# Kernel optimization log

Measured on AMD Instinct MI355X. Metric: run time of the kernel, lower is better.

The kernel has to match this reference:

```python
import jax, jax.numpy as jnp
import numpy as np

B, M, IN_DIM, D, H, NL = 4, 2048, 512, 1024, 4, 2
HD = D // H           # head_dim = 256
HD2 = HD // 2
ROPE_BASE = 10000.0
LN_EPS = 1e-5


def setup_inputs() -> dict:
    key = jax.random.key(0)
    ks = jax.random.split(key, 9)
    s = 0.02
    return {
        "x": jax.random.normal(ks[0], (B, M, IN_DIM), jnp.float32),
        "positions": jnp.sort(jax.random.randint(ks[1], (B, M), 0, 8192), axis=-1).astype(jnp.int32),
        "mask": jnp.ones((B, M), jnp.float32),
        "in_w": jax.random.normal(ks[2], (IN_DIM, D), jnp.float32) * s,
        "in_b": jnp.zeros((D,), jnp.float32),
        "qkv_w": jax.random.normal(ks[3], (NL, D, 3 * D), jnp.float32) * s,
        "o_w": jax.random.normal(ks[4], (NL, D, D), jnp.float32) * s,
        "ln1_g": jnp.ones((NL, D), jnp.float32),
        "ln1_b": jnp.zeros((NL, D), jnp.float32),
        "ffn_w1": jax.random.normal(ks[5], (NL, D, 4 * D), jnp.float32) * s,
        "ffn_b1": jnp.zeros((NL, 4 * D), jnp.float32),
        "ffn_w2": jax.random.normal(ks[6], (NL, 4 * D, D), jnp.float32) * s,
        "ffn_b2": jnp.zeros((NL, D), jnp.float32),
        "ln2_g": jnp.ones((NL, D), jnp.float32),
        "ln2_b": jnp.zeros((NL, D), jnp.float32),
        "start_state": jax.random.normal(ks[7], (D,), jnp.float32) * 0.02,
    }


def _layernorm(x, g, b):
    mu = jnp.mean(x, axis=-1, keepdims=True)
    var = jnp.mean((x - mu) ** 2, axis=-1, keepdims=True)
    return (x - mu) * jax.lax.rsqrt(var + LN_EPS) * g + b


def _rope_cos_sin(positions):
    # rope_module(pos): angles over head_dim//2 freqs, shared across heads
    inv_freq = 1.0 / (ROPE_BASE ** (jnp.arange(HD2, dtype=jnp.float32) * 2.0 / HD))
    ang = positions.astype(jnp.float32)[:, :, None] * inv_freq  # (B, L, HD2)
    return jnp.cos(ang), jnp.sin(ang)


def _apply_rotary(x, cos, sin):
    # x: (B, H, L, HD); cos/sin: (B, 1, L, HD2) broadcast over heads
    x1, x2 = x[..., :HD2], x[..., HD2:]
    return jnp.concatenate([x1 * cos - x2 * sin, x1 * sin + x2 * cos], axis=-1)


def _self_attention(x, cos, sin, mask, qkv_w, o_w):
    Bx, L, Dx = x.shape
    qkv = (x @ qkv_w).reshape(Bx, L, 3, H, HD)
    q = jnp.transpose(qkv[:, :, 0], (0, 2, 1, 3))  # (B, H, L, HD)
    k = jnp.transpose(qkv[:, :, 1], (0, 2, 1, 3))
    v = jnp.transpose(qkv[:, :, 2], (0, 2, 1, 3))
    q = _apply_rotary(q, cos, sin)
    k = _apply_rotary(k, cos, sin)
    scores = jnp.einsum("bhqd,bhkd->bhqk", q, k) * (1.0 / np.sqrt(HD))
    scores = jnp.where(mask[:, None, None, :] == 0, -jnp.inf, scores)
    attn = jax.nn.softmax(scores, axis=-1)
    out = jnp.einsum("bhqk,bhkd->bhqd", attn, v)
    out = jnp.transpose(out, (0, 2, 1, 3)).reshape(Bx, L, Dx)
    return out @ o_w


def reference(x, positions, mask, in_w, in_b, qkv_w, o_w, ln1_g, ln1_b,
              ffn_w1, ffn_b1, ffn_w2, ffn_b2, ln2_g, ln2_b, start_state):
    h = x @ in_w + in_b  # (B, M, D)
    cos, sin = _rope_cos_sin(positions)
    cos, sin = cos[:, None], sin[:, None]  # (B, 1, M, HD2)
    for l in range(NL):
        h = h + _self_attention(_layernorm(h, ln1_g[l], ln1_b[l]), cos, sin, mask,
                                qkv_w[l], o_w[l])
        y = _layernorm(h, ln2_g[l], ln2_b[l])
        y = jax.nn.gelu(y @ ffn_w1[l] + ffn_b1[l], approximate=False) @ ffn_w2[l] + ffn_b2[l]
        h = h + y
    lengths = jnp.sum(mask, axis=1)
    last_idx = jnp.clip(lengths.astype(jnp.int32) - 1, 0, None)
    gathered = h[jnp.arange(h.shape[0]), last_idx]  # (B, D)
    has_hist = lengths > 0
    return jnp.where(has_hist[:, None], gathered, start_state[None, :])
```

## Files before the change

### kernel.cpp

```cpp
#include <hip/hip_runtime.h>
#include <math.h>

typedef __attribute__((ext_vector_type(8))) short bf16x8;
typedef __attribute__((ext_vector_type(4))) float floatx4;
typedef __attribute__((ext_vector_type(4))) unsigned short ushort4v;

typedef __attribute__((address_space(1))) void as1_void;
typedef __attribute__((address_space(3))) void as3_void;

static __device__ __forceinline__ unsigned short f2b(float f) {
    union { float f; unsigned u; } v; v.f = f;
    unsigned r = v.u + 0x7fffu + ((v.u >> 16) & 1u);
    return (unsigned short)(r >> 16);
}
static __device__ __forceinline__ float b2f(unsigned short h) {
    union { unsigned u; float f; } v; v.u = ((unsigned)h) << 16;
    return v.f;
}

template<int T>
__global__ __launch_bounds__(256) void gemm_bf16(
    const unsigned short* __restrict__ A,
    const unsigned short* __restrict__ Bt,
    float* __restrict__ Cf, unsigned short* __restrict__ Cb,
    const float* __restrict__ bias,
    int K, int lda, int ldb, int ldc,
    int zdiv, long a_s1, long a_s2, long b_s1, long b_s2, long c_s1, long c_s2,
    int mode)
{
    constexpr int F  = T / 32;
    constexpr int NR = T / 64;

    __shared__ unsigned short As[3][4 * T * 8];
    __shared__ unsigned short Bs[3][4 * T * 8];

    const int tid  = threadIdx.x;
    const int wid  = tid >> 6;
    const int lane = tid & 63;
    const int q    = lane >> 4;
    const int r    = lane & 15;

    const int z  = blockIdx.z;
    const int zq = z / zdiv, zr = z % zdiv;
    const long offC = (long)zq * c_s1 + (long)zr * c_s2;

    const int m0 = blockIdx.y * T;
    const int n0 = blockIdx.x * T;

    const unsigned short* Ab = A  + (long)zq * a_s1 + (long)zr * a_s2 + (long)m0 * lda;
    const unsigned short* Bb = Bt + (long)zq * b_s1 + (long)zr * b_s2 + (long)n0 * ldb;

    const int wr = (wid >> 1) * (T / 2);
    const int wc = (wid & 1)  * (T / 2);

    floatx4 acc[F][F];
    #pragma unroll
    for (int i = 0; i < F; ++i)
        #pragma unroll
        for (int j = 0; j < F; ++j)
            acc[i][j] = (floatx4){0.f, 0.f, 0.f, 0.f};

    const int qc = wid;
    const int nk = K >> 5;

    auto stage = [&](int kt, int buf) {
        const int kofs = (kt << 5) + (qc << 3);
        #pragma unroll
        for (int rb = 0; rb < NR; ++rb)
            __builtin_amdgcn_global_load_lds(
                (as1_void*)(void*)(Ab + (long)(lane + rb * 64) * lda + kofs),
                (as3_void*)&As[buf][(qc * T + rb * 64) * 8], 16, 0, 0);
        #pragma unroll
        for (int rb = 0; rb < NR; ++rb)
            __builtin_amdgcn_global_load_lds(
                (as1_void*)(void*)(Bb + (long)(lane + rb * 64) * ldb + kofs),
                (as3_void*)&Bs[buf][(qc * T + rb * 64) * 8], 16, 0, 0);
    };

    stage(0, 0);
    if (nk > 1) stage(1, 1);

    int cur = 0, stb = 2;
    for (int kt = 0; kt < nk; ++kt) {
        if (kt + 1 < nk) {
            if constexpr (NR == 2) asm volatile("s_waitcnt vmcnt(4)" ::: "memory");
            else                   asm volatile("s_waitcnt vmcnt(2)" ::: "memory");
        } else {
            asm volatile("s_waitcnt vmcnt(0)" ::: "memory");
        }
        asm volatile("s_barrier" ::: "memory");
        if (kt + 2 < nk) stage(kt + 2, stb);

        bf16x8 av[F], bv[F];
        #pragma unroll
        for (int i = 0; i < F; ++i)
            av[i] = *(const bf16x8*)&As[cur][(q * T + wr + i * 16 + r) * 8];
        #pragma unroll
        for (int j = 0; j < F; ++j)
            bv[j] = *(const bf16x8*)&Bs[cur][(q * T + wc + j * 16 + r) * 8];
        #pragma unroll
        for (int i = 0; i < F; ++i)
            #pragma unroll
            for (int j = 0; j < F; ++j)
                acc[i][j] = __builtin_amdgcn_mfma_f32_16x16x32_bf16(av[i], bv[j], acc[i][j], 0, 0, 0);

        cur = (cur == 2) ? 0 : cur + 1;
        stb = (stb == 2) ? 0 : stb + 1;
    }

    #pragma unroll
    for (int i = 0; i < F; ++i) {
        const int gr0 = m0 + wr + i * 16 + q * 4;
        #pragma unroll
        for (int j = 0; j < F; ++j) {
            const int gc = n0 + wc + j * 16 + r;
            const float bvl = bias ? bias[gc] : 0.0f;
            #pragma unroll
            for (int rr = 0; rr < 4; ++rr) {
                const long cidx = offC + (long)(gr0 + rr) * ldc + gc;
                float v = acc[i][j][rr] + bvl;
                if (mode == 0) {
                    Cf[cidx] = v;
                } else if (mode == 1) {
                    Cf[cidx] += v;
                } else if (mode == 2) {
                    Cb[cidx] = f2b(v);
                } else {
                    Cb[cidx] = f2b(0.5f * v * (1.0f + erff(v * 0.70710678118654752f)));
                }
            }
        }
    }
}

__global__ void transpose_cast_f32(const float* __restrict__ in, unsigned short* __restrict__ out,
                                   int R, int C)
{
    __shared__ float t[32][33];
    const int c0 = blockIdx.x * 32, r0 = blockIdx.y * 32;
    const int tx = threadIdx.x, ty = threadIdx.y;
    #pragma unroll
    for (int i = 0; i < 4; ++i)
        t[ty + i * 8][tx] = in[(long)(r0 + ty + i * 8) * C + c0 + tx];
    __syncthreads();
    #pragma unroll
    for (int i = 0; i < 4; ++i)
        out[(long)(c0 + ty + i * 8) * R + r0 + tx] = f2b(t[tx][ty + i * 8]);
}

__global__ void transpose_v(const unsigned short* __restrict__ qkv, unsigned short* __restrict__ vT)
{
    __shared__ unsigned short t[32][33];
    const int hh = blockIdx.z;
    const int d0 = blockIdx.x * 32, m0 = blockIdx.y * 32;
    const int tx = threadIdx.x, ty = threadIdx.y;
    const unsigned short* ip = qkv + 2048 + hh * 256;
    unsigned short* op = vT + (long)hh * 524288;
    #pragma unroll
    for (int i = 0; i < 4; ++i)
        t[ty + i * 8][tx] = ip[(long)(m0 + ty + i * 8) * 3072 + d0 + tx];
    __syncthreads();
    #pragma unroll
    for (int i = 0; i < 4; ++i)
        op[(long)(d0 + ty + i * 8) * 2048 + m0 + tx] = t[tx][ty + i * 8];
}

__global__ void cast_f32_bf16(const float* __restrict__ in, unsigned short* __restrict__ out)
{
    const long i = (long)blockIdx.x * 256 + threadIdx.x;
    const float4 v = ((const float4*)in)[i];
    ushort4v o;
    o[0] = f2b(v.x); o[1] = f2b(v.y); o[2] = f2b(v.z); o[3] = f2b(v.w);
    ((ushort4v*)out)[i] = o;
}

__global__ void zero_f32(float* __restrict__ p)
{
    p[blockIdx.x * 256 + threadIdx.x] = 0.0f;
}

__global__ __launch_bounds__(256) void ln_kernel(const float* __restrict__ h,
    const float* __restrict__ g, const float* __restrict__ bta,
    unsigned short* __restrict__ out)
{
    const int tok = blockIdx.x;
    const float4 v = ((const float4*)(h + (long)tok * 1024))[threadIdx.x];
    float s  = v.x + v.y + v.z + v.w;
    float s2 = v.x * v.x + v.y * v.y + v.z * v.z + v.w * v.w;
    #pragma unroll
    for (int off = 32; off > 0; off >>= 1) {
        s  += __shfl_xor(s, off);
        s2 += __shfl_xor(s2, off);
    }
    __shared__ float rs[4], rs2[4];
    const int wid = threadIdx.x >> 6, lane = threadIdx.x & 63;
    if (lane == 0) { rs[wid] = s; rs2[wid] = s2; }
    __syncthreads();
    s  = rs[0] + rs[1] + rs[2] + rs[3];
    s2 = rs2[0] + rs2[1] + rs2[2] + rs2[3];
    const float mu = s * (1.0f / 1024.0f);
    float var = s2 * (1.0f / 1024.0f) - mu * mu;
    var = fmaxf(var, 0.0f);
    const float rsg = 1.0f / sqrtf(var + 1e-5f);
    const float4 gv = ((const float4*)g)[threadIdx.x];
    const float4 bv = ((const float4*)bta)[threadIdx.x];
    ushort4v o;
    o[0] = f2b((v.x - mu) * rsg * gv.x + bv.x);
    o[1] = f2b((v.y - mu) * rsg * gv.y + bv.y);
    o[2] = f2b((v.z - mu) * rsg * gv.z + bv.z);
    o[3] = f2b((v.w - mu) * rsg * gv.w + bv.w);
    *(ushort4v*)&out[(long)tok * 1024 + threadIdx.x * 4] = o;
}

__global__ __launch_bounds__(256) void rope_kernel(unsigned short* __restrict__ qkv,
                                                   const int* __restrict__ pos)
{
    const int tok = blockIdx.x;
    const float p = (float)pos[tok];
    unsigned short* base = qkv + (long)tok * 3072;
    #pragma unroll
    for (int it = 0; it < 2; ++it) {
        const int idx = threadIdx.x + it * 256;
        const int hh = idx >> 7, d = idx & 127;
        const float inv = powf(10000.0f, -(float)d * (1.0f / 128.0f));
        const float ang = p * inv;
        const float c = cosf(ang), s = sinf(ang);
        unsigned short* qp = base + hh * 256 + d;
        {
            const float x1 = b2f(qp[0]), x2 = b2f(qp[128]);
            qp[0]   = f2b(x1 * c - x2 * s);
            qp[128] = f2b(x1 * s + x2 * c);
        }
        unsigned short* kp = qp + 1024;
        {
            const float x1 = b2f(kp[0]), x2 = b2f(kp[128]);
            kp[0]   = f2b(x1 * c - x2 * s);
            kp[128] = f2b(x1 * s + x2 * c);
        }
    }
}

__global__ __launch_bounds__(256) void softmax_kernel(unsigned short* __restrict__ sc,
                                                      const float* __restrict__ mrow)
{
    unsigned short* row = sc + (long)blockIdx.x * 2048;
    const int t = threadIdx.x;

    float v[8];
    const ushort4v u0 = *(const ushort4v*)&row[t * 8];
    const ushort4v u1 = *(const ushort4v*)&row[t * 8 + 4];
    #pragma unroll
    for (int i = 0; i < 4; ++i) { v[i] = b2f(u0[i]); v[4 + i] = b2f(u1[i]); }

    float mx = -3.0e38f;
    #pragma unroll
    for (int i = 0; i < 8; ++i) {
        const float m = mrow[t * 8 + i];
        v[i] = (m == 0.0f) ? -3.0e38f : v[i] * 0.0625f;
        mx = fmaxf(mx, v[i]);
    }
    #pragma unroll
    for (int off = 32; off > 0; off >>= 1) mx = fmaxf(mx, __shfl_xor(mx, off));
    __shared__ float rmx[4], rsm[4];
    const int wid = t >> 6, lane = t & 63;
    if (lane == 0) rmx[wid] = mx;
    __syncthreads();
    mx = fmaxf(fmaxf(rmx[0], rmx[1]), fmaxf(rmx[2], rmx[3]));

    float s = 0.0f;
    #pragma unroll
    for (int i = 0; i < 8; ++i) { v[i] = expf(v[i] - mx); s += v[i]; }
    #pragma unroll
    for (int off = 32; off > 0; off >>= 1) s += __shfl_xor(s, off);
    if (lane == 0) rsm[wid] = s;
    __syncthreads();
    s = rsm[0] + rsm[1] + rsm[2] + rsm[3];
    const float invs = (s > 0.0f) ? 1.0f / s : 0.0f;

    ushort4v o0, o1;
    #pragma unroll
    for (int i = 0; i < 4; ++i) { o0[i] = f2b(v[i] * invs); o1[i] = f2b(v[4 + i] * invs); }
    *(ushort4v*)&row[t * 8]     = o0;
    *(ushort4v*)&row[t * 8 + 4] = o1;
}

__global__ __launch_bounds__(256) void gather_kernel(const float* __restrict__ h,
    const float* __restrict__ mask, const float* __restrict__ ss, float* __restrict__ out)
{
    const int b = blockIdx.x;
    const float* mrow = mask + b * 2048;
    const int t = threadIdx.x;
    float s = 0.0f;
    #pragma unroll
    for (int i = 0; i < 8; ++i) s += mrow[t * 8 + i];
    #pragma unroll
    for (int off = 32; off > 0; off >>= 1) s += __shfl_xor(s, off);
    __shared__ float red[4];
    if ((t & 63) == 0) red[t >> 6] = s;
    __syncthreads();
    const float len = red[0] + red[1] + red[2] + red[3];
    const int L = (int)len;
    const int last = (L > 0) ? (L - 1) : 0;
    const bool has = len > 0.0f;
    const float* src = has ? (h + ((long)b * 2048 + last) * 1024) : ss;
    #pragma unroll
    for (int i = 0; i < 4; ++i) {
        const int d = t + i * 256;
        out[b * 1024 + d] = src[d];
    }
}

extern "C" void kernel_launch(void* const* d_in, const int* in_sizes, int n_in,
                              void* d_out, int out_size, void* d_ws, size_t ws_size,
                              hipStream_t stream)
{
    (void)in_sizes; (void)n_in; (void)out_size;
    const float* x      = (const float*)d_in[0];
    const int*   pos    = (const int*)d_in[1];
    const float* mask   = (const float*)d_in[2];
    const float* in_w   = (const float*)d_in[3];
    const float* in_b   = (const float*)d_in[4];
    const float* qkv_w  = (const float*)d_in[5];
    const float* o_w    = (const float*)d_in[6];
    const float* ln1_g  = (const float*)d_in[7];
    const float* ln1_b  = (const float*)d_in[8];
    const float* ffn_w1 = (const float*)d_in[9];
    const float* ffn_b1 = (const float*)d_in[10];
    const float* ffn_w2 = (const float*)d_in[11];
    const float* ffn_b2 = (const float*)d_in[12];
    const float* ln2_g  = (const float*)d_in[13];
    const float* ln2_b  = (const float*)d_in[14];
    const float* sstate = (const float*)d_in[15];
    float* out = (float*)d_out;

    const size_t NEED = 143654912ull;
    if (ws_size < NEED) {
        zero_f32<<<16, 256, 0, stream>>>(out);
        return;
    }
    char* w = (char*)d_ws;
    unsigned short* wt_in  = (unsigned short*)(w);
    unsigned short* wt_qkv = (unsigned short*)(w + 1048576);
    unsigned short* wt_o   = (unsigned short*)(w + 7340032);
    unsigned short* wt_f1  = (unsigned short*)(w + 9437184);
    unsigned short* wt_f2  = (unsigned short*)(w + 17825792);
    float*          hbuf   = (float*)(w + 26214400);
    unsigned short* xn_bf  = (unsigned short*)(w + 59768832);
    unsigned short* ao_bf  = (unsigned short*)(w + 76546048);
    unsigned short* qkv_b  = (unsigned short*)(w + 93323264);
    unsigned short* vT_b   = (unsigned short*)(w + 105906176);
    unsigned short* scmid  = (unsigned short*)(w + 110100480);
    unsigned short* x_bf   = ao_bf;
    unsigned short* mid_bf = (unsigned short*)(w + 76546048);

    const dim3 tb(32, 8);

    transpose_cast_f32<<<dim3(32, 16), tb, 0, stream>>>(in_w, wt_in, 512, 1024);
    cast_f32_bf16<<<4096, 256, 0, stream>>>(x, x_bf);

    gemm_bf16<128><<<dim3(8, 64, 1), 256, 0, stream>>>(x_bf, wt_in, hbuf, nullptr, in_b,
        512, 512, 512, 1024, 1, 0, 0, 0, 0, 0, 0, 0);

    for (int l = 0; l < 2; ++l) {
        transpose_cast_f32<<<dim3(96, 32),  tb, 0, stream>>>(qkv_w  + (long)l * 3145728, wt_qkv, 1024, 3072);
        transpose_cast_f32<<<dim3(32, 32),  tb, 0, stream>>>(o_w    + (long)l * 1048576, wt_o,   1024, 1024);
        transpose_cast_f32<<<dim3(128, 32), tb, 0, stream>>>(ffn_w1 + (long)l * 4194304, wt_f1,  1024, 4096);
        transpose_cast_f32<<<dim3(32, 128), tb, 0, stream>>>(ffn_w2 + (long)l * 4194304, wt_f2,  4096, 1024);

        ln_kernel<<<8192, 256, 0, stream>>>(hbuf, ln1_g + l * 1024, ln1_b + l * 1024, xn_bf);

        for (int b = 0; b < 4; ++b) {
            gemm_bf16<64><<<dim3(48, 32, 1), 256, 0, stream>>>(xn_bf + (long)b * 2097152, wt_qkv,
                nullptr, qkv_b, nullptr, 1024, 1024, 1024, 3072, 1, 0, 0, 0, 0, 0, 0, 2);
            rope_kernel<<<2048, 256, 0, stream>>>(qkv_b, pos + b * 2048);
            transpose_v<<<dim3(8, 64, 4), tb, 0, stream>>>(qkv_b, vT_b);
            gemm_bf16<128><<<dim3(16, 16, 4), 256, 0, stream>>>(qkv_b, qkv_b + 1024,
                nullptr, scmid, nullptr, 256, 3072, 3072, 2048,
                1, 256l, 0, 256l, 0, 4194304l, 0, 2);
            softmax_kernel<<<8192, 256, 0, stream>>>(scmid, mask + b * 2048);
            gemm_bf16<64><<<dim3(4, 32, 4), 256, 0, stream>>>(scmid, vT_b,
                nullptr, ao_bf + (long)b * 2097152, nullptr, 2048, 2048, 2048, 1024,
                1, 4194304l, 0, 524288l, 0, 256l, 0, 2);
        }
        gemm_bf16<128><<<dim3(8, 64, 1), 256, 0, stream>>>(ao_bf, wt_o,
            hbuf, nullptr, nullptr, 1024, 1024, 1024, 1024, 1, 0, 0, 0, 0, 0, 0, 1);

        ln_kernel<<<8192, 256, 0, stream>>>(hbuf, ln2_g + l * 1024, ln2_b + l * 1024, xn_bf);

        gemm_bf16<128><<<dim3(32, 64, 1), 256, 0, stream>>>(xn_bf, wt_f1,
            nullptr, mid_bf, ffn_b1 + l * 4096, 1024, 1024, 1024, 4096, 1, 0, 0, 0, 0, 0, 0, 3);
        gemm_bf16<128><<<dim3(8, 64, 1), 256, 0, stream>>>(mid_bf, wt_f2,
            hbuf, nullptr, ffn_b2 + l * 1024, 4096, 4096, 4096, 1024, 1, 0, 0, 0, 0, 0, 0, 1);
    }

    gather_kernel<<<4, 256, 0, stream>>>(hbuf, mask, sstate, out);
}
```

Baseline: 2.275 ms.

## Double-buffer LDS fragment registers to overlap next-tile reads with MFMA

Restructures the GEMM main loop so the A/B fragments for the next k-tile are read from LDS into a second register set before the current tile's MFMAs run. The loop is unrolled by two so the two register sets alternate. The global-to-LDS stage for tile kt+2 is now issued before the wait and barrier, and an explicit lgkmcnt wait is added. The goal is to hide LDS read latency behind matrix instructions, at the cost of more registers. The loop also assumes an even number of k-tiles.

```diff
diff --git a/kernel.cpp b/kernel.cpp
--- a/kernel.cpp
+++ b/kernel.cpp
@@ -77,35 +77,49 @@
                 (as3_void*)&Bs[buf][(qc * T + rb * 64) * 8], 16, 0, 0);
     };
 
+    bf16x8 av0[F], bv0[F], av1[F], bv1[F];
+
     stage(0, 0);
     if (nk > 1) stage(1, 1);
-
-    int cur = 0, stb = 2;
-    for (int kt = 0; kt < nk; ++kt) {
+    if (nk > 1) { if constexpr (NR == 2) asm volatile("s_waitcnt vmcnt(4)" ::: "memory");
+                  else                   asm volatile("s_waitcnt vmcnt(2)" ::: "memory"); }
+    else          asm volatile("s_waitcnt vmcnt(0)" ::: "memory");
+    asm volatile("s_barrier" ::: "memory");
+    #pragma unroll
+    for (int i = 0; i < F; ++i) av0[i] = *(const bf16x8*)&As[0][(q * T + wr + i * 16 + r) * 8];
+    #pragma unroll
+    for (int j = 0; j < F; ++j) bv0[j] = *(const bf16x8*)&Bs[0][(q * T + wc + j * 16 + r) * 8];
+
+    auto body = [&](int kt, bf16x8 (&avc)[F], bf16x8 (&bvc)[F],
+                            bf16x8 (&avn)[F], bf16x8 (&bvn)[F]) {
+        if (kt + 2 < nk) stage(kt + 2, (kt + 2) % 3);
         if (kt + 1 < nk) {
-            if constexpr (NR == 2) asm volatile("s_waitcnt vmcnt(4)" ::: "memory");
-            else                   asm volatile("s_waitcnt vmcnt(2)" ::: "memory");
-        } else {
-            asm volatile("s_waitcnt vmcnt(0)" ::: "memory");
+            if (kt + 2 < nk) {
+                if constexpr (NR == 2) asm volatile("s_waitcnt vmcnt(4)" ::: "memory");
+                else                   asm volatile("s_waitcnt vmcnt(2)" ::: "memory");
+            } else {
+                asm volatile("s_waitcnt vmcnt(0)" ::: "memory");
+            }
+            asm volatile("s_waitcnt lgkmcnt(0)" ::: "memory");
+            asm volatile("s_barrier" ::: "memory");
+            const int bN = (kt + 1) % 3;
+            #pragma unroll
+            for (int i = 0; i < F; ++i)
+                avn[i] = *(const bf16x8*)&As[bN][(q * T + wr + i * 16 + r) * 8];
+            #pragma unroll
+            for (int j = 0; j < F; ++j)
+                bvn[j] = *(const bf16x8*)&Bs[bN][(q * T + wc + j * 16 + r) * 8];
         }
-        asm volatile("s_barrier" ::: "memory");
-        if (kt + 2 < nk) stage(kt + 2, stb);
-
-        bf16x8 av[F], bv[F];
-        #pragma unroll
-        for (int i = 0; i < F; ++i)
-            av[i] = *(const bf16x8*)&As[cur][(q * T + wr + i * 16 + r) * 8];
-        #pragma unroll
-        for (int j = 0; j < F; ++j)
-            bv[j] = *(const bf16x8*)&Bs[cur][(q * T + wc + j * 16 + r) * 8];
         #pragma unroll
         for (int i = 0; i < F; ++i)
             #pragma unroll
             for (int j = 0; j < F; ++j)
-                acc[i][j] = __builtin_amdgcn_mfma_f32_16x16x32_bf16(av[i], bv[j], acc[i][j], 0, 0, 0);
-
-        cur = (cur == 2) ? 0 : cur + 1;
-        stb = (stb == 2) ? 0 : stb + 1;
+                acc[i][j] = __builtin_amdgcn_mfma_f32_16x16x32_bf16(avc[i], bvc[j], acc[i][j], 0, 0, 0);
+    };
+
+    for (int kt = 0; kt < nk; kt += 2) {
+        body(kt,     av0, bv0, av1, bv1);
+        body(kt + 1, av1, bv1, av0, bv0);
     }
 
     #pragma unroll
```

Result: slower. 2.528 ms (+11.2%).
